# Performance work log

Hardware: AMD Instinct MI355X
Metric: run time of the kernel (lower is better)

The kernel has to match this reference:

```python
import jax, jax.numpy as jnp
import numpy as np

NH, HD = 16, 64  # num_heads, head_size (hidden=1024)
LN_EPS = 1e-5


def setup_inputs() -> dict:
    key = jax.random.key(0)
    ks = jax.random.split(key, 8)
    B, SQ, SKV, H = 4, 16, 8192, NH * HD
    return {
        "x": jax.random.normal(ks[0], (B, SQ, H), jnp.float32),
        "x_mass": jax.random.normal(ks[1], (B, SQ, 1, HD), jnp.float32),
        "k_cache": jax.random.normal(ks[2], (B, NH, SKV, HD), jnp.float32),
        "v_cache": jax.random.normal(ks[3], (B, NH, SKV, HD), jnp.float32),
        "wq": jax.random.normal(ks[4], (H, H), jnp.float32) * (1.0 / np.sqrt(H)),
        "bq": jnp.zeros((H,), jnp.float32),
        "wo": jax.random.normal(ks[5], (H, H), jnp.float32) * (1.0 / np.sqrt(H)),
        "bo": jnp.zeros((H,), jnp.float32),
        "gamma": jnp.ones((H,), jnp.float32),
        "beta": jnp.zeros((H,), jnp.float32),
    }


def _apply_rope(q, dis):
    # q: [B,Sq,NH,HD], dis: [B,Sq,1,HD]
    dis_sin, dis_cos = jnp.split(dis, 2, axis=-1)
    q0, q1 = jnp.split(q, 2, axis=-1)
    return jnp.concatenate([q0 * dis_cos - q1 * dis_sin,
                            q0 * dis_sin + q1 * dis_cos], axis=-1)


def reference(x, x_mass, k_cache, v_cache, wq, bq, wo, bo, gamma, beta):
    B, SQ, H = x.shape
    q = (x @ wq.T + bq).reshape(B, SQ, NH, HD)
    q = _apply_rope(q, x_mass)                      # [B,Sq,NH,HD]
    # SDPA with scale=1 (module passes scale=1 explicitly)
    scores = jnp.einsum('bqhd,bhkd->bhqk', q, k_cache)
    attn = jax.nn.softmax(scores, axis=-1)
    ctx = jnp.einsum('bhqk,bhkd->bqhd', attn, v_cache).reshape(B, SQ, H)
    postx = ctx @ wo.T + bo
    y = x + postx
    mu = jnp.mean(y, axis=-1, keepdims=True)
    var = jnp.var(y, axis=-1, keepdims=True)
    return (y - mu) * jax.lax.rsqrt(var + LN_EPS) * gamma + beta
```

## Files before the change

### kernel.cpp

```cpp
#include <hip/hip_runtime.h>
#include <math.h>

#define NHEADS 16
#define HD 64
#define HID 1024
#define BATCH 4
#define SQ 16
#define SKV 8192
#define ROWS 64
#define NCHUNK 32
#define CHUNK 256
#define LN_EPS 1e-5f

typedef _Float16 half4v __attribute__((ext_vector_type(4)));
typedef _Float16 half8v __attribute__((ext_vector_type(8)));
typedef float f32x4 __attribute__((ext_vector_type(4)));

__global__ __launch_bounds__(256) void qrope_gemv(
    const float* __restrict__ x,
    const float* __restrict__ xm,
    const float* __restrict__ wq,
    const float* __restrict__ bq,
    float* __restrict__ qout)
{
    __shared__ float xs[ROWS * 256];
    __shared__ float sqx[4][ROWS];

    const int t = threadIdx.x, w = t >> 6, l = t & 63;
    const int cb = blockIdx.x;
    const int h = cb >> 4;
    const int sub = cb & 15;
    const int dd = sub * 2 + (w & 1) + (w >> 1) * 32;
    const int j = h * 64 + dd;

    float acc[ROWS];
    #pragma unroll
    for (int r = 0; r < ROWS; ++r) acc[r] = 0.f;

    const float4* x4 = (const float4*)x;
    const float4* w4 = (const float4*)(wq + (size_t)j * HID);
    float4* xs4 = (float4*)xs;

    for (int ck = 0; ck < 4; ++ck) {
        __syncthreads();
        #pragma unroll
        for (int p = 0; p < 16; ++p) {
            const int idx = t + p * 256;
            const int r = idx >> 6, c = idx & 63;
            xs4[idx] = x4[(size_t)r * 256 + ck * 64 + c];
        }
        __syncthreads();

        const float4 wf = w4[ck * 64 + l];
        #pragma unroll
        for (int r = 0; r < ROWS; ++r) {
            const float4 xf = xs4[r * 64 + l];
            acc[r] += wf.x * xf.x + wf.y * xf.y + wf.z * xf.z + wf.w * xf.w;
        }
    }

    #pragma unroll
    for (int r = 0; r < ROWS; ++r) {
        float a = acc[r];
        #pragma unroll
        for (int off = 32; off; off >>= 1) a += __shfl_xor(a, off);
        acc[r] = a;
    }
    float val = acc[0];
    #pragma unroll
    for (int r = 1; r < ROWS; ++r) val = (l == r) ? acc[r] : val;
    val += bq[j];

    sqx[w][l] = val;
    __syncthreads();

    const int r = l;
    float outv;
    if (w < 2) {
        const float q0 = sqx[w][l];
        const float q1 = sqx[w + 2][l];
        const float sn = xm[r * 64 + dd];
        const float co = xm[r * 64 + 32 + dd];
        outv = q0 * co - q1 * sn;
    } else {
        const int d2 = dd - 32;
        const float q0 = sqx[w - 2][l];
        const float q1 = sqx[w][l];
        const float sn = xm[r * 64 + d2];
        const float co = xm[r * 64 + 32 + d2];
        outv = q0 * sn + q1 * co;
    }
    const int b = r >> 4, s_ = r & 15;
    qout[(((size_t)b * NHEADS + h) * SQ + s_) * HD + dd] = outv;
}

__global__ __launch_bounds__(256, 2) void attn_partial(
    const float* __restrict__ q,
    const float* __restrict__ kc,
    const float* __restrict__ vc,
    float* __restrict__ o_part,
    float* __restrict__ ml_part)
{
    __shared__ _Float16 Ks[4][64 * 64];
    __shared__ float pL[4][SQ][68];
    __shared__ float mL[4][SQ];
    __shared__ float lL[4][SQ];

    const int chunk = blockIdx.x, h = blockIdx.y, b = blockIdx.z;
    const int bh = b * NHEADS + h;
    const int t = threadIdx.x, w = t >> 6, l = t & 63;
    const int lo = l & 15, g = l >> 4;

    const size_t kvbase = (size_t)bh * SKV * HD + ((size_t)chunk * CHUNK + w * 64) * HD;
    const float4* kb = (const float4*)(kc + kvbase);
    const float* vb = vc + kvbase;
    const float* qb = q + (size_t)bh * SQ * HD;

    _Float16* ks = Ks[w];
    #pragma unroll
    for (int p = 0; p < 16; ++p) {
        const int fidx = p * 64 + l;
        const float4 kv = kb[fidx];
        const int row = fidx >> 4, c4 = fidx & 15;
        const int byteoff = (row * 128 + c4 * 8) ^ ((row & 7) << 4);
        half4v hv = { (_Float16)kv.x, (_Float16)kv.y, (_Float16)kv.z, (_Float16)kv.w };
        *(half4v*)((char*)ks + byteoff) = hv;
    }

    half8v bQ[2];
    #pragma unroll
    for (int kk = 0; kk < 2; ++kk) {
        const float4 qa = *(const float4*)(qb + lo * HD + kk * 32 + g * 8);
        const float4 qc = *(const float4*)(qb + lo * HD + kk * 32 + g * 8 + 4);
        bQ[kk] = (half8v){ (_Float16)qa.x, (_Float16)qa.y, (_Float16)qa.z, (_Float16)qa.w,
                           (_Float16)qc.x, (_Float16)qc.y, (_Float16)qc.z, (_Float16)qc.w };
    }

    f32x4 S[4];
    #pragma unroll
    for (int kg = 0; kg < 4; ++kg) {
        f32x4 acc = {0.f, 0.f, 0.f, 0.f};
        #pragma unroll
        for (int kk = 0; kk < 2; ++kk) {
            const int row = kg * 16 + lo;
            const int byteoff = (row * 128 + kk * 64 + g * 16) ^ ((row & 7) << 4);
            const half8v aK = *(const half8v*)((const char*)ks + byteoff);
            acc = __builtin_amdgcn_mfma_f32_16x16x32_f16(aK, bQ[kk], acc, 0, 0, 0);
        }
        S[kg] = acc;
    }

    float mx = S[0][0];
    #pragma unroll
    for (int kg = 0; kg < 4; ++kg)
        #pragma unroll
        for (int r = 0; r < 4; ++r) mx = fmaxf(mx, S[kg][r]);
    mx = fmaxf(mx, __shfl_xor(mx, 16));
    mx = fmaxf(mx, __shfl_xor(mx, 32));

    float ls = 0.f;
    #pragma unroll
    for (int kg = 0; kg < 4; ++kg) {
        #pragma unroll
        for (int r = 0; r < 4; ++r) {
            const float pe = __expf(S[kg][r] - mx);
            ls += pe;
            pL[w][lo][kg * 16 + g * 4 + r] = pe;
        }
    }
    ls += __shfl_xor(ls, 16);
    ls += __shfl_xor(ls, 32);
    if (g == 0) { mL[w][lo] = mx; lL[w][lo] = ls; }

    f32x4 oacc[SQ];
    #pragma unroll
    for (int r = 0; r < SQ; ++r) oacc[r] = (f32x4){0.f, 0.f, 0.f, 0.f};

    #pragma unroll
    for (int k4 = 0; k4 < 4; ++k4) {
        float4 vv[4];
        #pragma unroll
        for (int j = 0; j < 4; ++j)
            vv[j] = *(const float4*)(vb + (size_t)(g * 16 + k4 * 4 + j) * HD + lo * 4);
        #pragma unroll
        for (int r = 0; r < SQ; ++r) {
            const f32x4 p4 = *(const f32x4*)&pL[w][r][g * 16 + k4 * 4];
            oacc[r][0] += p4[0] * vv[0].x + p4[1] * vv[1].x + p4[2] * vv[2].x + p4[3] * vv[3].x;
            oacc[r][1] += p4[0] * vv[0].y + p4[1] * vv[1].y + p4[2] * vv[2].y + p4[3] * vv[3].y;
            oacc[r][2] += p4[0] * vv[0].z + p4[1] * vv[1].z + p4[2] * vv[2].z + p4[3] * vv[3].z;
            oacc[r][3] += p4[0] * vv[0].w + p4[1] * vv[1].w + p4[2] * vv[2].w + p4[3] * vv[3].w;
        }
    }

    #pragma unroll
    for (int r = 0; r < SQ; ++r) {
        #pragma unroll
        for (int off = 16; off <= 32; off <<= 1) {
            oacc[r][0] += __shfl_xor(oacc[r][0], off);
            oacc[r][1] += __shfl_xor(oacc[r][1], off);
            oacc[r][2] += __shfl_xor(oacc[r][2], off);
            oacc[r][3] += __shfl_xor(oacc[r][3], off);
        }
    }

    if (g == 0) {
        #pragma unroll
        for (int r = 0; r < SQ; ++r)
            *(f32x4*)&pL[w][r][lo * 4] = oacc[r];
    }
    __syncthreads();

    {
        const int r = t >> 4, dq = t & 15;
        const float M = fmaxf(fmaxf(mL[0][r], mL[1][r]), fmaxf(mL[2][r], mL[3][r]));
        float L = 0.f;
        f32x4 O = (f32x4){0.f, 0.f, 0.f, 0.f};
        #pragma unroll
        for (int ww = 0; ww < 4; ++ww) {
            const float sc = __expf(mL[ww][r] - M);
            L += lL[ww][r] * sc;
            const f32x4 ov = *(const f32x4*)&pL[ww][r][dq * 4];
            O[0] += ov[0] * sc; O[1] += ov[1] * sc; O[2] += ov[2] * sc; O[3] += ov[3] * sc;
        }
        *(f32x4*)(o_part + (((size_t)bh * NCHUNK + chunk) * SQ + r) * HD + dq * 4) = O;
        if (dq == 0) {
            ml_part[(((size_t)bh * NCHUNK + chunk) * SQ + r) * 2 + 0] = M;
            ml_part[(((size_t)bh * NCHUNK + chunk) * SQ + r) * 2 + 1] = L;
        }
    }
}

__global__ __launch_bounds__(256) void attn_combine(
    const float* __restrict__ o_part,
    const float* __restrict__ ml_part,
    float* __restrict__ ctx)
{
    __shared__ float mls[NCHUNK * 4 * 2];
    const int bh = blockIdx.x >> 2, qg = blockIdx.x & 3;
    const int b = bh >> 4, h = bh & 15;
    const int t = threadIdx.x;
    const int qi_l = t >> 6, d = t & 63;
    const int qi = qg * 4 + qi_l;

    mls[t] = ml_part[(((size_t)bh * NCHUNK + (t >> 3)) * SQ + qg * 4 + ((t >> 1) & 3)) * 2 + (t & 1)];
    __syncthreads();

    float M = -INFINITY;
    #pragma unroll
    for (int c = 0; c < NCHUNK; ++c) M = fmaxf(M, mls[(c * 4 + qi_l) * 2]);
    float L = 0.f, O = 0.f;
    #pragma unroll 4
    for (int c = 0; c < NCHUNK; ++c) {
        const float sc = __expf(mls[(c * 4 + qi_l) * 2] - M);
        L += mls[(c * 4 + qi_l) * 2 + 1] * sc;
        O += o_part[(((size_t)bh * NCHUNK + c) * SQ + qi) * HD + d] * sc;
    }
    ctx[((size_t)(b * SQ + qi)) * HID + h * HD + d] = O / L;
}

__global__ __launch_bounds__(256) void out_gemv(
    const float* __restrict__ ctx,
    const float* __restrict__ x,
    const float* __restrict__ wo,
    const float* __restrict__ bo,
    float* __restrict__ y)
{
    __shared__ float xs[ROWS * 256];

    const int t = threadIdx.x, w = t >> 6, l = t & 63;
    const int j = blockIdx.x * 4 + w;

    float acc[ROWS];
    #pragma unroll
    for (int r = 0; r < ROWS; ++r) acc[r] = 0.f;

    const float4* c4 = (const float4*)ctx;
    const float4* w4 = (const float4*)(wo + (size_t)j * HID);
    float4* xs4 = (float4*)xs;

    for (int ck = 0; ck < 4; ++ck) {
        __syncthreads();
        #pragma unroll
        for (int p = 0; p < 16; ++p) {
            const int idx = t + p * 256;
            const int r = idx >> 6, c = idx & 63;
            xs4[idx] = c4[(size_t)r * 256 + ck * 64 + c];
        }
        __syncthreads();

        const float4 wf = w4[ck * 64 + l];
        #pragma unroll
        for (int r = 0; r < ROWS; ++r) {
            const float4 xf = xs4[r * 64 + l];
            acc[r] += wf.x * xf.x + wf.y * xf.y + wf.z * xf.z + wf.w * xf.w;
        }
    }

    #pragma unroll
    for (int r = 0; r < ROWS; ++r) {
        float a = acc[r];
        #pragma unroll
        for (int off = 32; off; off >>= 1) a += __shfl_xor(a, off);
        acc[r] = a;
    }
    float val = acc[0];
    #pragma unroll
    for (int r = 1; r < ROWS; ++r) val = (l == r) ? acc[r] : val;

    val += bo[j] + x[(size_t)l * HID + j];
    y[(size_t)l * HID + j] = val;
}

__global__ __launch_bounds__(256) void ln_kernel(
    const float* __restrict__ y,
    const float* __restrict__ gamma,
    const float* __restrict__ beta,
    float* __restrict__ out)
{
    __shared__ float red[8];
    const int r = blockIdx.x, t = threadIdx.x;
    const int w = t >> 6, l = t & 63;

    const float4 yv = ((const float4*)(y + (size_t)r * HID))[t];
    float sum = yv.x + yv.y + yv.z + yv.w;
    float ssq = yv.x * yv.x + yv.y * yv.y + yv.z * yv.z + yv.w * yv.w;
    #pragma unroll
    for (int off = 32; off; off >>= 1) {
        sum += __shfl_xor(sum, off);
        ssq += __shfl_xor(ssq, off);
    }
    if (l == 0) { red[w] = sum; red[4 + w] = ssq; }
    __syncthreads();
    sum = red[0] + red[1] + red[2] + red[3];
    ssq = red[4] + red[5] + red[6] + red[7];
    const float mu = sum * (1.f / HID);
    const float var = ssq * (1.f / HID) - mu * mu;
    const float rstd = rsqrtf(var + LN_EPS);

    const float4 g = ((const float4*)gamma)[t];
    const float4 be = ((const float4*)beta)[t];
    float4 o;
    o.x = (yv.x - mu) * rstd * g.x + be.x;
    o.y = (yv.y - mu) * rstd * g.y + be.y;
    o.z = (yv.z - mu) * rstd * g.z + be.z;
    o.w = (yv.w - mu) * rstd * g.w + be.w;
    ((float4*)(out + (size_t)r * HID))[t] = o;
}

extern "C" void kernel_launch(void* const* d_in, const int* in_sizes, int n_in,
                              void* d_out, int out_size, void* d_ws, size_t ws_size,
                              hipStream_t stream) {
    const float* x     = (const float*)d_in[0];
    const float* xm    = (const float*)d_in[1];
    const float* kc    = (const float*)d_in[2];
    const float* vc    = (const float*)d_in[3];
    const float* wq    = (const float*)d_in[4];
    const float* bq    = (const float*)d_in[5];
    const float* wo    = (const float*)d_in[6];
    const float* bo    = (const float*)d_in[7];
    const float* gamma = (const float*)d_in[8];
    const float* beta  = (const float*)d_in[9];
    float* out = (float*)d_out;

    float* ws = (float*)d_ws;
    float* q_ws   = ws;
    float* o_ws   = q_ws + ROWS * HID;
    float* ml_ws  = o_ws + (size_t)BATCH * NHEADS * NCHUNK * SQ * HD;
    float* ctx_ws = ml_ws + BATCH * NHEADS * NCHUNK * SQ * 2;
    float* y_ws   = ctx_ws + ROWS * HID;

    qrope_gemv<<<dim3(256), 256, 0, stream>>>(x, xm, wq, bq, q_ws);
    attn_partial<<<dim3(NCHUNK, NHEADS, BATCH), 256, 0, stream>>>(q_ws, kc, vc, o_ws, ml_ws);
    attn_combine<<<dim3(256), 256, 0, stream>>>(o_ws, ml_ws, ctx_ws);
    out_gemv<<<dim3(256), 256, 0, stream>>>(ctx_ws, x, wo, bo, y_ws);
    ln_kernel<<<dim3(ROWS), 256, 0, stream>>>(y_ws, gamma, beta, out);
}
```

Before: 116.1 us.

## Software-pipeline K/V global loads and halve K shared buffer in attn_partial

Splits each wave's 64-row K tile into two 32-row halves staged through a smaller shared buffer, issuing the second half's global loads while the first half's MFMA scores run. V rows for the PV step are prefetched early into two double-buffered register sets, so the loads overlap the K work and earlier PV steps. The per-wave output is written into the reused K buffer instead of the pL region. This aims to hide global memory latency and cut LDS use to allow more occupancy, at the cost of more live registers (kreg, vA, vB) and a possible spill risk under the two-block launch bound.

```diff
diff --git a/kernel.cpp b/kernel.cpp
--- a/kernel.cpp
+++ b/kernel.cpp
@@ -94,6 +94,22 @@
     qout[(((size_t)b * NHEADS + h) * SQ + s_) * HD + dd] = outv;
 }
 
+#define PVSTEP(vX, k4)                                                         \
+    {                                                                          \
+        _Pragma("unroll")                                                      \
+        for (int r = 0; r < SQ; ++r) {                                         \
+            const f32x4 p4 = *(const f32x4*)&pL[w][r][g * 16 + (k4) * 4];      \
+            oacc[r][0] += p4[0] * vX[0].x + p4[1] * vX[1].x                    \
+                        + p4[2] * vX[2].x + p4[3] * vX[3].x;                   \
+            oacc[r][1] += p4[0] * vX[0].y + p4[1] * vX[1].y                    \
+                        + p4[2] * vX[2].y + p4[3] * vX[3].y;                   \
+            oacc[r][2] += p4[0] * vX[0].z + p4[1] * vX[1].z                    \
+                        + p4[2] * vX[2].z + p4[3] * vX[3].z;                   \
+            oacc[r][3] += p4[0] * vX[0].w + p4[1] * vX[1].w                    \
+                        + p4[2] * vX[2].w + p4[3] * vX[3].w;                   \
+        }                                                                      \
+    }
+
 __global__ __launch_bounds__(256, 2) void attn_partial(
     const float* __restrict__ q,
     const float* __restrict__ kc,
@@ -101,7 +117,7 @@
     float* __restrict__ o_part,
     float* __restrict__ ml_part)
 {
-    __shared__ _Float16 Ks[4][64 * 64];
+    __shared__ _Float16 Ks[4][32 * 64];
     __shared__ float pL[4][SQ][68];
     __shared__ float mL[4][SQ];
     __shared__ float lL[4][SQ];
@@ -116,16 +132,17 @@
     const float* vb = vc + kvbase;
     const float* qb = q + (size_t)bh * SQ * HD;
 
-    _Float16* ks = Ks[w];
-    #pragma unroll
-    for (int p = 0; p < 16; ++p) {
-        const int fidx = p * 64 + l;
-        const float4 kv = kb[fidx];
-        const int row = fidx >> 4, c4 = fidx & 15;
-        const int byteoff = (row * 128 + c4 * 8) ^ ((row & 7) << 4);
-        half4v hv = { (_Float16)kv.x, (_Float16)kv.y, (_Float16)kv.z, (_Float16)kv.w };
-        *(half4v*)((char*)ks + byteoff) = hv;
-    }
+    float4 kreg[8];
+    #pragma unroll
+    for (int p = 0; p < 8; ++p) kreg[p] = kb[p * 64 + l];
+
+    float4 vA[4], vB[4];
+    #pragma unroll
+    for (int j = 0; j < 4; ++j)
+        vA[j] = *(const float4*)(vb + (size_t)(g * 16 + j) * HD + lo * 4);
+    #pragma unroll
+    for (int j = 0; j < 4; ++j)
+        vB[j] = *(const float4*)(vb + (size_t)(g * 16 + 4 + j) * HD + lo * 4);
 
     half8v bQ[2];
     #pragma unroll
@@ -136,9 +153,23 @@
                            (_Float16)qc.x, (_Float16)qc.y, (_Float16)qc.z, (_Float16)qc.w };
     }
 
+    _Float16* ks = Ks[w];
+
+    #pragma unroll
+    for (int p = 0; p < 8; ++p) {
+        const int fidx = p * 64 + l;
+        const int row = fidx >> 4, c4 = fidx & 15;
+        const int byteoff = (row * 128 + c4 * 8) ^ ((row & 7) << 4);
+        half4v hv = { (_Float16)kreg[p].x, (_Float16)kreg[p].y,
+                      (_Float16)kreg[p].z, (_Float16)kreg[p].w };
+        *(half4v*)((char*)ks + byteoff) = hv;
+    }
+    #pragma unroll
+    for (int p = 0; p < 8; ++p) kreg[p] = kb[512 + p * 64 + l];
+
     f32x4 S[4];
     #pragma unroll
-    for (int kg = 0; kg < 4; ++kg) {
+    for (int kg = 0; kg < 2; ++kg) {
         f32x4 acc = {0.f, 0.f, 0.f, 0.f};
         #pragma unroll
         for (int kk = 0; kk < 2; ++kk) {
@@ -150,6 +181,29 @@
         S[kg] = acc;
     }
 
+    #pragma unroll
+    for (int p = 0; p < 8; ++p) {
+        const int fidx = p * 64 + l;
+        const int row = fidx >> 4, c4 = fidx & 15;
+        const int byteoff = (row * 128 + c4 * 8) ^ ((row & 7) << 4);
+        half4v hv = { (_Float16)kreg[p].x, (_Float16)kreg[p].y,
+                      (_Float16)kreg[p].z, (_Float16)kreg[p].w };
+        *(half4v*)((char*)ks + byteoff) = hv;
+    }
+
+    #pragma unroll
+    for (int kg = 2; kg < 4; ++kg) {
+        f32x4 acc = {0.f, 0.f, 0.f, 0.f};
+        #pragma unroll
+        for (int kk = 0; kk < 2; ++kk) {
+            const int row = (kg - 2) * 16 + lo;
+            const int byteoff = (row * 128 + kk * 64 + g * 16) ^ ((row & 7) << 4);
+            const half8v aK = *(const half8v*)((const char*)ks + byteoff);
+            acc = __builtin_amdgcn_mfma_f32_16x16x32_f16(aK, bQ[kk], acc, 0, 0, 0);
+        }
+        S[kg] = acc;
+    }
+
     float mx = S[0][0];
     #pragma unroll
     for (int kg = 0; kg < 4; ++kg)
@@ -176,21 +230,16 @@
     #pragma unroll
     for (int r = 0; r < SQ; ++r) oacc[r] = (f32x4){0.f, 0.f, 0.f, 0.f};
 
-    #pragma unroll
-    for (int k4 = 0; k4 < 4; ++k4) {
-        float4 vv[4];
-        #pragma unroll
-        for (int j = 0; j < 4; ++j)
-            vv[j] = *(const float4*)(vb + (size_t)(g * 16 + k4 * 4 + j) * HD + lo * 4);
-        #pragma unroll
-        for (int r = 0; r < SQ; ++r) {
-            const f32x4 p4 = *(const f32x4*)&pL[w][r][g * 16 + k4 * 4];
-            oacc[r][0] += p4[0] * vv[0].x + p4[1] * vv[1].x + p4[2] * vv[2].x + p4[3] * vv[3].x;
-            oacc[r][1] += p4[0] * vv[0].y + p4[1] * vv[1].y + p4[2] * vv[2].y + p4[3] * vv[3].y;
-            oacc[r][2] += p4[0] * vv[0].z + p4[1] * vv[1].z + p4[2] * vv[2].z + p4[3] * vv[3].z;
-            oacc[r][3] += p4[0] * vv[0].w + p4[1] * vv[1].w + p4[2] * vv[2].w + p4[3] * vv[3].w;
-        }
-    }
+    PVSTEP(vA, 0);
+    #pragma unroll
+    for (int j = 0; j < 4; ++j)
+        vA[j] = *(const float4*)(vb + (size_t)(g * 16 + 8 + j) * HD + lo * 4);
+    PVSTEP(vB, 1);
+    #pragma unroll
+    for (int j = 0; j < 4; ++j)
+        vB[j] = *(const float4*)(vb + (size_t)(g * 16 + 12 + j) * HD + lo * 4);
+    PVSTEP(vA, 2);
+    PVSTEP(vB, 3);
 
     #pragma unroll
     for (int r = 0; r < SQ; ++r) {
@@ -203,10 +252,11 @@
         }
     }
 
+    float* oW = (float*)Ks[w];
     if (g == 0) {
         #pragma unroll
         for (int r = 0; r < SQ; ++r)
-            *(f32x4*)&pL[w][r][lo * 4] = oacc[r];
+            *(f32x4*)&oW[r * 64 + lo * 4] = oacc[r];
     }
     __syncthreads();
 
@@ -219,7 +269,7 @@
         for (int ww = 0; ww < 4; ++ww) {
             const float sc = __expf(mL[ww][r] - M);
             L += lL[ww][r] * sc;
-            const f32x4 ov = *(const f32x4*)&pL[ww][r][dq * 4];
+            const f32x4 ov = *(const f32x4*)&((const float*)Ks[ww])[r * 64 + dq * 4];
             O[0] += ov[0] * sc; O[1] += ov[1] * sc; O[2] += ov[2] * sc; O[3] += ov[3] * sc;
         }
         *(f32x4*)(o_part + (((size_t)bh * NCHUNK + chunk) * SQ + r) * HD + dq * 4) = O;
```

Result: slower. 188.1 us (+62.1%).

## Split attention chunk across eight waves with 32 keys each and batched K loads

Applied to the files above, without the earlier changes.

Doubles the waves per attention block from 4 to 8, each handling 32 keys instead of 64, so more loads are in flight per CU. All eight K float4 loads now go into registers before any conversion and LDS write, and the P buffer is shrunk and written as vectors. Per-wave partial outputs reuse the K shared buffer, and the cross-wave combine merges 8 partials. The cost is a larger block, a longer reduction and more register pressure under the 512-thread, 4-block launch bound.

```diff
diff --git a/kernel.cpp b/kernel.cpp
--- a/kernel.cpp
+++ b/kernel.cpp
@@ -10,6 +10,8 @@
 #define ROWS 64
 #define NCHUNK 32
 #define CHUNK 256
+#define WAVES 8
+#define KEYSW 32
 #define LN_EPS 1e-5f
 
 typedef _Float16 half4v __attribute__((ext_vector_type(4)));
@@ -94,38 +96,31 @@
     qout[(((size_t)b * NHEADS + h) * SQ + s_) * HD + dd] = outv;
 }
 
-__global__ __launch_bounds__(256, 2) void attn_partial(
+__global__ __launch_bounds__(512, 4) void attn_partial(
     const float* __restrict__ q,
     const float* __restrict__ kc,
     const float* __restrict__ vc,
     float* __restrict__ o_part,
     float* __restrict__ ml_part)
 {
-    __shared__ _Float16 Ks[4][64 * 64];
-    __shared__ float pL[4][SQ][68];
-    __shared__ float mL[4][SQ];
-    __shared__ float lL[4][SQ];
+    __shared__ _Float16 Ks[WAVES][KEYSW * 64];
+    __shared__ float pL[WAVES][SQ * 36];
+    __shared__ float mL[WAVES][SQ];
+    __shared__ float lL[WAVES][SQ];
 
     const int chunk = blockIdx.x, h = blockIdx.y, b = blockIdx.z;
     const int bh = b * NHEADS + h;
     const int t = threadIdx.x, w = t >> 6, l = t & 63;
     const int lo = l & 15, g = l >> 4;
 
-    const size_t kvbase = (size_t)bh * SKV * HD + ((size_t)chunk * CHUNK + w * 64) * HD;
+    const size_t kvbase = (size_t)bh * SKV * HD + ((size_t)chunk * CHUNK + w * KEYSW) * HD;
     const float4* kb = (const float4*)(kc + kvbase);
     const float* vb = vc + kvbase;
     const float* qb = q + (size_t)bh * SQ * HD;
 
-    _Float16* ks = Ks[w];
-    #pragma unroll
-    for (int p = 0; p < 16; ++p) {
-        const int fidx = p * 64 + l;
-        const float4 kv = kb[fidx];
-        const int row = fidx >> 4, c4 = fidx & 15;
-        const int byteoff = (row * 128 + c4 * 8) ^ ((row & 7) << 4);
-        half4v hv = { (_Float16)kv.x, (_Float16)kv.y, (_Float16)kv.z, (_Float16)kv.w };
-        *(half4v*)((char*)ks + byteoff) = hv;
-    }
+    float4 kreg[8];
+    #pragma unroll
+    for (int p = 0; p < 8; ++p) kreg[p] = kb[p * 64 + l];
 
     half8v bQ[2];
     #pragma unroll
@@ -136,9 +131,21 @@
                            (_Float16)qc.x, (_Float16)qc.y, (_Float16)qc.z, (_Float16)qc.w };
     }
 
-    f32x4 S[4];
-    #pragma unroll
-    for (int kg = 0; kg < 4; ++kg) {
+    _Float16* ks = Ks[w];
+
+    #pragma unroll
+    for (int p = 0; p < 8; ++p) {
+        const int fidx = p * 64 + l;
+        const int row = fidx >> 4, c4 = fidx & 15;
+        const int byteoff = (row * 128 + c4 * 8) ^ ((row & 7) << 4);
+        half4v hv = { (_Float16)kreg[p].x, (_Float16)kreg[p].y,
+                      (_Float16)kreg[p].z, (_Float16)kreg[p].w };
+        *(half4v*)((char*)ks + byteoff) = hv;
+    }
+
+    f32x4 S[2];
+    #pragma unroll
+    for (int kg = 0; kg < 2; ++kg) {
         f32x4 acc = {0.f, 0.f, 0.f, 0.f};
         #pragma unroll
         for (int kk = 0; kk < 2; ++kk) {
@@ -152,7 +159,7 @@
 
     float mx = S[0][0];
     #pragma unroll
-    for (int kg = 0; kg < 4; ++kg)
+    for (int kg = 0; kg < 2; ++kg)
         #pragma unroll
         for (int r = 0; r < 4; ++r) mx = fmaxf(mx, S[kg][r]);
     mx = fmaxf(mx, __shfl_xor(mx, 16));
@@ -160,13 +167,14 @@
 
     float ls = 0.f;
     #pragma unroll
-    for (int kg = 0; kg < 4; ++kg) {
+    for (int kg = 0; kg < 2; ++kg) {
+        f32x4 pq;
         #pragma unroll
         for (int r = 0; r < 4; ++r) {
-            const float pe = __expf(S[kg][r] - mx);
-            ls += pe;
-            pL[w][lo][kg * 16 + g * 4 + r] = pe;
-        }
+            pq[r] = __expf(S[kg][r] - mx);
+            ls += pq[r];
+        }
+        *(f32x4*)&pL[w][lo * 36 + kg * 16 + g * 4] = pq;
     }
     ls += __shfl_xor(ls, 16);
     ls += __shfl_xor(ls, 32);
@@ -177,14 +185,14 @@
     for (int r = 0; r < SQ; ++r) oacc[r] = (f32x4){0.f, 0.f, 0.f, 0.f};
 
     #pragma unroll
-    for (int k4 = 0; k4 < 4; ++k4) {
+    for (int k4 = 0; k4 < 2; ++k4) {
         float4 vv[4];
         #pragma unroll
         for (int j = 0; j < 4; ++j)
-            vv[j] = *(const float4*)(vb + (size_t)(g * 16 + k4 * 4 + j) * HD + lo * 4);
+            vv[j] = *(const float4*)(vb + (size_t)(g * 8 + k4 * 4 + j) * HD + lo * 4);
         #pragma unroll
         for (int r = 0; r < SQ; ++r) {
-            const f32x4 p4 = *(const f32x4*)&pL[w][r][g * 16 + k4 * 4];
+            const f32x4 p4 = *(const f32x4*)&pL[w][r * 36 + g * 8 + k4 * 4];
             oacc[r][0] += p4[0] * vv[0].x + p4[1] * vv[1].x + p4[2] * vv[2].x + p4[3] * vv[3].x;
             oacc[r][1] += p4[0] * vv[0].y + p4[1] * vv[1].y + p4[2] * vv[2].y + p4[3] * vv[3].y;
             oacc[r][2] += p4[0] * vv[0].z + p4[1] * vv[1].z + p4[2] * vv[2].z + p4[3] * vv[3].z;
@@ -203,23 +211,26 @@
         }
     }
 
+    float* oW = (float*)Ks[w];
     if (g == 0) {
         #pragma unroll
         for (int r = 0; r < SQ; ++r)
-            *(f32x4*)&pL[w][r][lo * 4] = oacc[r];
+            *(f32x4*)&oW[r * 64 + lo * 4] = oacc[r];
     }
     __syncthreads();
 
-    {
+    if (t < 256) {
         const int r = t >> 4, dq = t & 15;
-        const float M = fmaxf(fmaxf(mL[0][r], mL[1][r]), fmaxf(mL[2][r], mL[3][r]));
+        float M = mL[0][r];
+        #pragma unroll
+        for (int ww = 1; ww < WAVES; ++ww) M = fmaxf(M, mL[ww][r]);
         float L = 0.f;
         f32x4 O = (f32x4){0.f, 0.f, 0.f, 0.f};
         #pragma unroll
-        for (int ww = 0; ww < 4; ++ww) {
+        for (int ww = 0; ww < WAVES; ++ww) {
             const float sc = __expf(mL[ww][r] - M);
             L += lL[ww][r] * sc;
-            const f32x4 ov = *(const f32x4*)&pL[ww][r][dq * 4];
+            const f32x4 ov = *(const f32x4*)&((const float*)Ks[ww])[r * 64 + dq * 4];
             O[0] += ov[0] * sc; O[1] += ov[1] * sc; O[2] += ov[2] * sc; O[3] += ov[3] * sc;
         }
         *(f32x4*)(o_part + (((size_t)bh * NCHUNK + chunk) * SQ + r) * HD + dq * 4) = O;
@@ -370,7 +381,7 @@
     float* y_ws   = ctx_ws + ROWS * HID;
 
     qrope_gemv<<<dim3(256), 256, 0, stream>>>(x, xm, wq, bq, q_ws);
-    attn_partial<<<dim3(NCHUNK, NHEADS, BATCH), 256, 0, stream>>>(q_ws, kc, vc, o_ws, ml_ws);
+    attn_partial<<<dim3(NCHUNK, NHEADS, BATCH), 512, 0, stream>>>(q_ws, kc, vc, o_ws, ml_ws);
     attn_combine<<<dim3(256), 256, 0, stream>>>(o_ws, ml_ws, ctx_ws);
     out_gemv<<<dim3(256), 256, 0, stream>>>(ctx_ws, x, wo, bo, y_ws);
     ln_kernel<<<dim3(ROWS), 256, 0, stream>>>(y_ws, gamma, beta, out);
```

Result: slower. 224.4 us (+93.3%).
